# Optimization experiments

Hardware: AMD Instinct MI355X
Metric: run time of the kernel (lower is better)

## Reference

```python
import jax, jax.numpy as jnp
import numpy as np

B_SZ, L, D_MODEL = 8, 4096, 64
D_INNER, D_STATE, DT_RANK, K = 128, 16, 4, 4  # expand=2, d_state=16, dt_rank=ceil(64/16), d_conv=4


def setup_inputs() -> dict:
    key = jax.random.key(0)
    ks = jax.random.split(key, 8)
    r = lambda k, sh, s=0.02: jax.random.normal(k, sh, dtype=jnp.float32) * s
    A_init = jnp.log(jnp.arange(1, D_STATE + 1, dtype=jnp.float32))  # S4D-real init
    return {
        "x": jax.random.normal(ks[0], (B_SZ, L, D_MODEL), dtype=jnp.float32),
        "ln_g": jnp.ones((D_MODEL,), jnp.float32),
        "ln_b": jnp.zeros((D_MODEL,), jnp.float32),
        "in_proj_w": r(ks[1], (2, 2 * D_INNER, D_MODEL)),
        "conv_w": r(ks[2], (2, D_INNER, K), 0.1),
        "conv_b": jnp.zeros((2, D_INNER), jnp.float32),
        "x_proj_w": r(ks[3], (2, DT_RANK + 2 * D_STATE, D_INNER)),
        "dt_proj_w": r(ks[4], (2, D_INNER, DT_RANK), 0.1),
        "dt_bias": jnp.full((2, D_INNER), -4.0, jnp.float32) + r(ks[5], (2, D_INNER), 0.1),
        "A_log": jnp.broadcast_to(A_init, (2, D_INNER, D_STATE)) + 0.0,
        "D": jnp.ones((2, D_INNER), jnp.float32),
        "out_proj_w": r(ks[6], (2, D_MODEL, D_INNER)),
    }


def _mamba(x, in_w, cw, cb, xp_w, dtp_w, dtb, A_log, Dp, out_w):
    # x: [B, L, d_model] -> [B, L, d_model]
    xz = x @ in_w.T                         # [B, L, 2*d_inner]
    xi, z = jnp.split(xz, 2, axis=-1)
    # causal depthwise conv1d, kernel K, left-pad K-1
    xi_c = jnp.transpose(xi, (0, 2, 1))     # [B, d_inner, L]
    xi_c = jax.lax.conv_general_dilated(
        xi_c, cw[:, None, :], (1,), [(K - 1, 0)],
        dimension_numbers=("NCH", "OIH", "NCH"), feature_group_count=D_INNER)
    xi = jax.nn.silu(jnp.transpose(xi_c, (0, 2, 1)) + cb)  # [B, L, d_inner]
    xdb = xi @ xp_w.T                       # [B, L, dt_rank + 2*N]
    dt_low, Bm, C = jnp.split(xdb, [DT_RANK, DT_RANK + D_STATE], axis=-1)
    dt = jax.nn.softplus(dt_low @ dtp_w.T + dtb)  # [B, L, d_inner]
    A = -jnp.exp(A_log)                     # [d_inner, N]

    def step(h, inp):
        xt, dtt, Bt, Ct = inp               # [B,d], [B,d], [B,N], [B,N]
        dA = jnp.exp(dtt[..., None] * A)    # [B, d, N]
        h = dA * h + (dtt * xt)[..., None] * Bt[:, None, :]
        return h, jnp.einsum("bdn,bn->bd", h, Ct)

    h0 = jnp.zeros((x.shape[0], D_INNER, D_STATE), x.dtype)
    seq = (jnp.swapaxes(xi, 0, 1), jnp.swapaxes(dt, 0, 1),
           jnp.swapaxes(Bm, 0, 1), jnp.swapaxes(C, 0, 1))
    _, ys = jax.lax.scan(step, h0, seq)
    y = jnp.swapaxes(ys, 0, 1) + xi * Dp    # D skip connection
    y = y * jax.nn.silu(z)                  # gate
    return y @ out_w.T                      # [B, L, d_model]


def reference(x, ln_g, ln_b, in_proj_w, conv_w, conv_b, x_proj_w, dt_proj_w, dt_bias, A_log, D, out_proj_w):
    mu = jnp.mean(x, axis=-1, keepdims=True)
    var = jnp.var(x, axis=-1, keepdims=True)
    xn = (x - mu) * jax.lax.rsqrt(var + 1e-5) * ln_g + ln_b
    p = lambda i: (in_proj_w[i], conv_w[i], conv_b[i], x_proj_w[i], dt_proj_w[i],
                   dt_bias[i], A_log[i], D[i], out_proj_w[i])
    y_fwd = _mamba(xn, *p(0))
    y_bwd = jnp.flip(_mamba(jnp.flip(xn, axis=1), *p(1)), axis=1)
    return y_fwd + y_bwd
```

## Files before the change

### kernel.cpp

```cpp
#include <hip/hip_runtime.h>

#define Bsz 8
#define Lx 4096
#define DM 64
#define DI 128
#define NS 16
#define RK 4
#define KC 4
#define NC 64
#define CT 64

typedef __attribute__((ext_vector_type(8))) __bf16 bf16x8v;
typedef __attribute__((ext_vector_type(4))) __bf16 bf16x4v;
typedef __attribute__((ext_vector_type(4))) float f32x4;

__device__ __forceinline__ float fsig(float x){ return 1.f/(1.f+__expf(-x)); }
__device__ __forceinline__ float dot4(float4 a, float4 b){
  return fmaf(a.x,b.x, fmaf(a.y,b.y, fmaf(a.z,b.z, a.w*b.w)));
}
__device__ __forceinline__ void pow8(float e1, int half, float p[8]){
  float e2=e1*e1, e4=e2*e2, e8=e4*e4;
  if (half){
    p[0]=e8*e1; p[1]=e8*e2; p[2]=p[1]*e1; p[3]=e8*e4;
    p[4]=p[3]*e1; p[5]=p[3]*e2; p[6]=p[5]*e1; p[7]=e8*e8;
  } else {
    p[0]=e1; p[1]=e2; p[2]=e2*e1; p[3]=e4;
    p[4]=e4*e1; p[5]=e4*e2; p[6]=p[5]*e1; p[7]=e8;
  }
}

__global__ __launch_bounds__(512) void a1_front(
    const float* __restrict__ x, const float* __restrict__ ln_g, const float* __restrict__ ln_b,
    const float* __restrict__ in_w, const float* __restrict__ conv_w, const float* __restrict__ conv_b,
    const float* __restrict__ xp_w, const float* __restrict__ dtp_w, const float* __restrict__ dt_b,
    float* __restrict__ xcg, float* __restrict__ dtg, float* __restrict__ zg,
    float* __restrict__ Bg, float* __restrict__ Cg)
{
  __shared__ float uA[4864];
  __shared__ float uB[8192];
  const int tid = threadIdx.x;
  const int bx = blockIdx.x;
  const int tile = bx & 63;
  const int i = (bx >> 6) & 1;
  const int b = bx >> 7;
  const int l0 = tile * 64;
  const size_t rbase = (size_t)(b*2+i)*Lx + l0;

  {
    const int wv8 = tid >> 6, lane = tid & 63;
    const float gg = ln_g[lane], bb = ln_b[lane];
    for (int lr = wv8; lr < 67; lr += 8) {
      float v = 0.f;
      int l = l0 - 3 + lr;
      if (l >= 0) {
        int pl = i ? (Lx-1-l) : l;
        v = x[((size_t)b*Lx + pl)*DM + lane];
        float s = v, s2 = v*v;
        #pragma unroll
        for (int off=32; off; off>>=1){ s += __shfl_xor(s,off); s2 += __shfl_xor(s2,off); }
        float mu = s * (1.f/DM);
        float rs = rsqrtf(s2*(1.f/DM) - mu*mu + 1e-5f);
        v = (v-mu)*rs*gg + bb;
      }
      *(__bf16*)((char*)uA + ((lr*128 + lane*2) ^ ((lr&7)<<4))) = (__bf16)v;
    }
    #pragma unroll
    for (int it=0; it<8; ++it) {
      int g = it*512 + tid;
      int c = g >> 4, q = g & 15;
      float4 w = *(const float4*)(in_w + ((size_t)(i*2*DI) + c)*DM + q*4);
      bf16x4v hv;
      hv[0]=(__bf16)w.x; hv[1]=(__bf16)w.y; hv[2]=(__bf16)w.z; hv[3]=(__bf16)w.w;
      *(bf16x4v*)((char*)uB + ((c*128 + q*8) ^ ((c&7)<<4))) = hv;
    }
  }
  __syncthreads();

  const int lane = tid & 63, wv = tid >> 6;
  f32x4 acc[5][2];
  {
    f32x4 z4 = {0.f, 0.f, 0.f, 0.f};
    #pragma unroll
    for (int mt=0; mt<5; ++mt){ acc[mt][0] = z4; acc[mt][1] = z4; }
    bf16x8v bfr[2][2];
    #pragma unroll
    for (int ntl=0; ntl<2; ++ntl)
      #pragma unroll
      for (int kt=0; kt<2; ++kt){
        int c = (wv*2+ntl)*16 + (lane&15);
        int byt = (c*128 + kt*64 + (lane>>4)*16) ^ ((c&7)<<4);
        bfr[ntl][kt] = *(const bf16x8v*)((const char*)uB + byt);
      }
    #pragma unroll
    for (int mt=0; mt<5; ++mt){
      bf16x8v afr[2];
      #pragma unroll
      for (int kt=0; kt<2; ++kt){
        int row = mt*16 + (lane&15);
        int byt = (row*128 + kt*64 + (lane>>4)*16) ^ ((row&7)<<4);
        afr[kt] = *(const bf16x8v*)((const char*)uA + byt);
      }
      #pragma unroll
      for (int ntl=0; ntl<2; ++ntl){
        acc[mt][ntl] = __builtin_amdgcn_mfma_f32_16x16x32_bf16(afr[0], bfr[ntl][0], acc[mt][ntl], 0,0,0);
        acc[mt][ntl] = __builtin_amdgcn_mfma_f32_16x16x32_bf16(afr[1], bfr[ntl][1], acc[mt][ntl], 0,0,0);
      }
    }
  }
  __syncthreads();

  {
    const int d = tid & 127, rh = tid >> 7;
    const float4 cw = *(const float4*)(conv_w + (size_t)(i*DI + d)*KC);
    const float cb = conv_b[i*DI + d];
    #pragma unroll
    for (int h=0; h<2; ++h) {
      if (wv < 4) {
        #pragma unroll
        for (int mt=0; mt<5; ++mt)
          #pragma unroll
          for (int ntl=0; ntl<2; ++ntl)
            #pragma unroll
            for (int r=0; r<4; ++r){
              int m = mt*16 + (lane>>4)*4 + r;
              if (m >= h*32 && m <= h*32+34)
                uA[(m - h*32)*129 + wv*32 + ntl*16 + (lane&15)] = acc[mt][ntl][r];
            }
      } else if (h == 0) {
        #pragma unroll
        for (int mt=0; mt<5; ++mt)
          #pragma unroll
          for (int ntl=0; ntl<2; ++ntl)
            #pragma unroll
            for (int r=0; r<4; ++r){
              int m = mt*16 + (lane>>4)*4 + r;
              if (m >= 3 && m <= 66)
                zg[(rbase + (m-3))*DI + (wv-4)*32 + ntl*16 + (lane&15)] = acc[mt][ntl][r];
            }
      }
      __syncthreads();
      #pragma unroll
      for (int rr=0; rr<8; ++rr){
        int r = h*32 + rh*8 + rr;
        int lb = rh*8 + rr;
        float v0 = uA[(lb  )*129 + d];
        float v1 = uA[(lb+1)*129 + d];
        float v2 = uA[(lb+2)*129 + d];
        float v3 = uA[(lb+3)*129 + d];
        float aa = cb + cw.x*v0 + cw.y*v1 + cw.z*v2 + cw.w*v3;
        float xc = aa * fsig(aa);
        xcg[(rbase + r)*DI + d] = xc;
        __bf16 hh = (__bf16)xc;
        __bf16 ll = (__bf16)(xc - (float)hh);
        int off = (r*256 + d*2) ^ ((r&7)<<4);
        *(__bf16*)((char*)uB + off) = hh;
        *(__bf16*)((char*)uB + off + 16384) = ll;
      }
      __syncthreads();
    }
  }

  for (int e = tid; e < 36*32; e += 512) {
    int j = e >> 5, k0 = (e & 31)*4;
    float4 w = *(const float4*)(xp_w + ((size_t)(i*36) + j)*DI + k0);
    float vv[4] = {w.x, w.y, w.z, w.w};
    bf16x4v hv, lv;
    #pragma unroll
    for (int k=0;k<4;++k){
      __bf16 hh = (__bf16)vv[k];
      hv[k] = hh;
      lv[k] = (__bf16)(vv[k] - (float)hh);
    }
    int off = (j*256 + k0*2) ^ ((j&7)<<4);
    *(bf16x4v*)((char*)uA + off) = hv;
    *(bf16x4v*)((char*)uA + off + 9216) = lv;
  }
  __syncthreads();

  for (int t = wv; t < 12; t += 8) {
    int mt = t & 3, nt = t >> 2;
    f32x4 a2 = {0.f,0.f,0.f,0.f};
    #pragma unroll
    for (int kt=0; kt<4; ++kt){
      int row = mt*16 + (lane&15);
      int ab = (row*256 + kt*64 + (lane>>4)*16) ^ ((row&7)<<4);
      bf16x8v ah = *(const bf16x8v*)((const char*)uB + ab);
      bf16x8v al = *(const bf16x8v*)((const char*)uB + ab + 16384);
      int col = nt*16 + (lane&15);
      int bby = (col*256 + kt*64 + (lane>>4)*16) ^ ((col&7)<<4);
      bf16x8v bh = *(const bf16x8v*)((const char*)uA + bby);
      bf16x8v bl = *(const bf16x8v*)((const char*)uA + bby + 9216);
      a2 = __builtin_amdgcn_mfma_f32_16x16x32_bf16(ah, bh, a2, 0,0,0);
      a2 = __builtin_amdgcn_mfma_f32_16x16x32_bf16(al, bh, a2, 0,0,0);
      a2 = __builtin_amdgcn_mfma_f32_16x16x32_bf16(ah, bl, a2, 0,0,0);
    }
    #pragma unroll
    for (int rg4=0; rg4<4; ++rg4){
      int row = mt*16 + (lane>>4)*4 + rg4;
      int j = nt*16 + (lane&15);
      float val = a2[rg4];
      if (j < 4) uA[4608 + row*4 + j] = val;
      else if (j < 20) Bg[(rbase+row)*NS + (j-4)] = val;
      else if (j < 36) Cg[(rbase+row)*NS + (j-20)] = val;
    }
  }
  __syncthreads();

  #pragma unroll 4
  for (int it=0; it<16; ++it) {
    int e = it*512 + tid;
    int r = e >> 7, d = e & 127;
    float4 dl = *(const float4*)&uA[4608 + r*4];
    float4 w  = *(const float4*)(dtp_w + (size_t)(i*DI + d)*RK);
    float a = dt_b[i*DI + d] + dot4(w, dl);
    dtg[(rbase + r)*DI + d] = (a > 15.f) ? a : __logf(1.f + __expf(a));
  }
}

__global__ __launch_bounds__(256) void ks_scan(
    float* dtg, float* xcg,
    const float* __restrict__ Bg, const float* __restrict__ Cg,
    const float* __restrict__ A_log, const float* __restrict__ Dp,
    float* __restrict__ Pm, float* __restrict__ hend)
{
  __shared__ float sB[CT*NS];
  __shared__ float sC[CT*NS];
  const int tid = threadIdx.x;
  const int bx = blockIdx.x;
  const int c = bx % NC; const int i = (bx/NC)&1; const int b = bx/(2*NC);
  const int d = tid >> 1, half = tid & 1, n0 = half*8;
  const size_t rb = ((size_t)(b*2+i)*Lx + (size_t)c*CT);
  ((float4*)sB)[tid] = ((const float4*)(Bg + rb*NS))[tid];
  ((float4*)sC)[tid] = ((const float4*)(Cg + rb*NS))[tid];
  float a[8], h[8];
  bool afast = true;
  #pragma unroll
  for (int n=0;n<8;++n){
    a[n] = -__expf(A_log[((size_t)(i*DI)+d)*NS + n0+n]);
    float tgt = (float)(n0+n+1);
    afast = afast && (fabsf(a[n] + tgt) <= 1e-4f*tgt);
    h[n] = 0.f;
  }
  const float Dd = Dp[i*DI + d];
  float S = 0.f;
  float dt4[4], x4[4];
  #pragma unroll
  for (int k=0;k<4;++k){
    size_t g = (rb + k)*DI + d;
    dt4[k] = dtg[g];
    x4[k]  = xcg[g];
  }
  __syncthreads();
  for (int r4 = 0; r4 < CT; r4 += 4){
    float dtn[4], xn[4];
    if (r4 + 4 < CT){
      #pragma unroll
      for (int k=0;k<4;++k){
        size_t g = (rb + r4 + 4 + k)*DI + d;
        dtn[k] = dtg[g];
        xn[k]  = xcg[g];
      }
    }
    #pragma unroll
    for (int k=0;k<4;++k){
      float dtt = dt4[k];
      float xcv = x4[k];
      float u = dtt * xcv;
      S += dtt;
      const float* bp = &sB[(r4 + k)*NS + n0];
      const float* cp = &sC[(r4 + k)*NS + n0];
      float4 b0 = *(const float4*)bp;
      float4 b1 = *(const float4*)(bp+4);
      float4 c0 = *(const float4*)cp;
      float4 c1 = *(const float4*)(cp+4);
      float bb[8] = {b0.x,b0.y,b0.z,b0.w,b1.x,b1.y,b1.z,b1.w};
      float cc[8] = {c0.x,c0.y,c0.z,c0.w,c1.x,c1.y,c1.z,c1.w};
      float pA = 0.f, pB = 0.f;
      if (afast){
        float p[8];
        pow8(__expf(-dtt), half, p);
        #pragma unroll
        for (int n=0;n<8;++n){
          h[n] = fmaf(p[n], h[n], u*bb[n]);
          if (n & 1) pB = fmaf(h[n], cc[n], pB); else pA = fmaf(h[n], cc[n], pA);
        }
      } else {
        #pragma unroll
        for (int n=0;n<8;++n){
          float dA = __expf(a[n]*dtt);
          h[n] = fmaf(dA, h[n], u*bb[n]);
          if (n & 1) pB = fmaf(h[n], cc[n], pB); else pA = fmaf(h[n], cc[n], pA);
        }
      }
      float part = pA + pB;
      float y = part + __shfl_xor(part, 1);
      if (half == 0){
        size_t g = (rb + r4 + k)*DI + d;
        dtg[g] = fmaf(xcv, Dd, y);
        xcg[g] = S;
      }
    }
    if (r4 + 4 < CT){
      #pragma unroll
      for (int k=0;k<4;++k){ dt4[k] = dtn[k]; x4[k] = xn[k]; }
    }
  }
  size_t ob = (((size_t)(b*2+i)*NC + c)*DI + d)*NS + n0;
  if (afast){
    float p[8];
    pow8(__expf(-S), half, p);
    #pragma unroll
    for (int n=0;n<8;++n) Pm[ob+n] = p[n];
  } else {
    #pragma unroll
    for (int n=0;n<8;++n) Pm[ob+n] = __expf(a[n]*S);
  }
  #pragma unroll
  for (int n=0;n<8;++n) hend[ob+n] = h[n];
}

__global__ __launch_bounds__(256) void kc_pass2(
    float* __restrict__ Pm, const float* __restrict__ hend)
{
  const int tid = threadIdx.x;
  const int bi = blockIdx.x;
  const int d = tid>>1, n0 = (tid&1)*8;
  float h[8];
  #pragma unroll
  for (int n=0;n<8;++n) h[n]=0.f;
  const size_t stride = (size_t)DI*NS;
  size_t ob = (((size_t)bi*NC)*DI + d)*NS + n0;
  float4 pa = *(const float4*)&Pm[ob],   pb = *(const float4*)&Pm[ob+4];
  float4 ea = *(const float4*)&hend[ob], eb = *(const float4*)&hend[ob+4];
  for (int c=0; c<NC; ++c){
    size_t obn = ob + stride;
    float4 qa=pa, qb=pb, fa=ea, fb=eb;
    if (c+1 < NC){
      qa = *(const float4*)&Pm[obn];   qb = *(const float4*)&Pm[obn+4];
      fa = *(const float4*)&hend[obn]; fb = *(const float4*)&hend[obn+4];
    }
    *(float4*)&Pm[ob]   = make_float4(h[0],h[1],h[2],h[3]);
    *(float4*)&Pm[ob+4] = make_float4(h[4],h[5],h[6],h[7]);
    h[0]=fmaf(pa.x,h[0],ea.x); h[1]=fmaf(pa.y,h[1],ea.y);
    h[2]=fmaf(pa.z,h[2],ea.z); h[3]=fmaf(pa.w,h[3],ea.w);
    h[4]=fmaf(pb.x,h[4],eb.x); h[5]=fmaf(pb.y,h[5],eb.y);
    h[6]=fmaf(pb.z,h[6],eb.z); h[7]=fmaf(pb.w,h[7],eb.w);
    pa=qa; pb=qb; ea=fa; eb=fb; ob = obn;
  }
}

__global__ __launch_bounds__(256) void ke_out(
    const float* __restrict__ yg, const float* __restrict__ Sg,
    const float* __restrict__ zg, const float* __restrict__ Cg,
    const float* __restrict__ h0g, const float* __restrict__ A_log,
    const float* __restrict__ ow, float* __restrict__ out)
{
  __shared__ char sY[16384];
  __shared__ char sW[16384];
  int* s_af = (int*)sW;
  const int tid = threadIdx.x;
  const int bx = blockIdx.x;
  const int tile = bx & 127; const int b = bx >> 7;
  const int l0 = tile * 32;
  const int q = tid & 31, rg = tid >> 5;
  if (tid < 2) s_af[tid] = 1;
  bool bad0 = false, bad1 = false;
  #pragma unroll
  for (int it=0; it<8; ++it){
    int e = it*256 + tid;
    int n = e & 15;
    float tgt = (float)(n+1);
    float a0 = __expf(A_log[e]);
    float a1 = __expf(A_log[DI*NS + e]);
    if (fabsf(a0 - tgt) > 1e-4f*tgt) bad0 = true;
    if (fabsf(a1 - tgt) > 1e-4f*tgt) bad1 = true;
  }
  __syncthreads();
  if (bad0) s_af[0] = 0;
  if (bad1) s_af[1] = 0;
  __syncthreads();
  const bool af0 = (s_af[0] != 0), af1 = (s_af[1] != 0);
  #pragma unroll
  for (int dir=0; dir<2; ++dir){
    const size_t strm = (size_t)(b*2+dir);
    const int cch = dir ? ((Lx-1-l0)>>6) : (l0>>6);
    const bool afast = dir ? af1 : af0;
    float h0q[4][16];
    #pragma unroll
    for (int dd=0; dd<4; ++dd)
      #pragma unroll
      for (int k=0;k<4;++k)
        *(float4*)&h0q[dd][k*4] =
            *(const float4*)&h0g[(((strm*NC) + cch)*DI + (q*4+dd))*NS + k*4];
    #pragma unroll
    for (int it=0; it<4; ++it){
      int r = it*8 + rg;
      size_t prow = strm*Lx + (size_t)(dir ? (Lx-1-(l0+r)) : (l0+r));
      float4 y4 = *(const float4*)&yg[prow*DI + q*4];
      float4 S4 = *(const float4*)&Sg[prow*DI + q*4];
      float4 z4 = *(const float4*)&zg[prow*DI + q*4];
      float c16[16];
      #pragma unroll
      for (int k=0;k<4;++k) *(float4*)&c16[k*4] = *(const float4*)&Cg[prow*NS + k*4];
      float yv[4] = {y4.x,y4.y,y4.z,y4.w};
      float Sv[4] = {S4.x,S4.y,S4.z,S4.w};
      float zv[4] = {z4.x,z4.y,z4.z,z4.w};
      bf16x4v hv;
      #pragma unroll
      for (int dd=0; dd<4; ++dd){
        float corr;
        if (afast){
          float e1 = __expf(-Sv[dd]);
          float g[16];
          #pragma unroll
          for (int n=0;n<16;++n) g[n] = c16[n]*h0q[dd][n];
          float t = g[15];
          #pragma unroll
          for (int n=14;n>=0;--n) t = fmaf(t, e1, g[n]);
          corr = t * e1;
        } else {
          corr = 0.f;
          #pragma unroll
          for (int n=0;n<16;++n){
            float an = -__expf(A_log[((size_t)(dir*DI) + q*4+dd)*NS + n]);
            corr = fmaf(__expf(an*Sv[dd])*c16[n], h0q[dd][n], corr);
          }
        }
        float zz = zv[dd];
        float yf = (yv[dd] + corr) * (zz * fsig(zz));
        hv[dd] = (__bf16)yf;
      }
      *(bf16x4v*)(sY + ((r*512 + dir*256 + q*8) ^ ((r&7)<<4))) = hv;
    }
  }
  __syncthreads();
  const int lane = tid & 63, wv = tid >> 6;
  f32x4 acc2[2] = {{0.f,0.f,0.f,0.f},{0.f,0.f,0.f,0.f}};
  #pragma unroll
  for (int dir=0; dir<2; ++dir){
    #pragma unroll
    for (int it=0; it<8; ++it){
      int e = it*256 + tid;
      int c = e >> 5, qq = e & 31;
      float4 w = *(const float4*)(ow + ((size_t)(dir*DM + c))*DI + qq*4);
      bf16x4v hv; hv[0]=(__bf16)w.x; hv[1]=(__bf16)w.y; hv[2]=(__bf16)w.z; hv[3]=(__bf16)w.w;
      *(bf16x4v*)(sW + ((c*256 + qq*8) ^ ((c&7)<<4))) = hv;
    }
    __syncthreads();
    #pragma unroll
    for (int t=0; t<2; ++t){
      int T = wv*2 + t, mt = T >> 2, nt = T & 3;
      #pragma unroll
      for (int ktl=0; ktl<4; ++ktl){
        int row = mt*16 + (lane&15);
        bf16x8v av = *(const bf16x8v*)(sY + ((row*512 + dir*256 + ktl*64 + (lane>>4)*16) ^ ((row&7)<<4)));
        int ch = nt*16 + (lane&15);
        bf16x8v wvv = *(const bf16x8v*)(sW + ((ch*256 + ktl*64 + (lane>>4)*16) ^ ((ch&7)<<4)));
        acc2[t] = __builtin_amdgcn_mfma_f32_16x16x32_bf16(av, wvv, acc2[t], 0,0,0);
      }
    }
    __syncthreads();
  }
  #pragma unroll
  for (int t=0; t<2; ++t){
    int T = wv*2 + t, mt = T >> 2, nt = T & 3;
    #pragma unroll
    for (int r=0; r<4; ++r){
      int m = mt*16 + (lane>>4)*4 + r;
      int ch = nt*16 + (lane&15);
      out[((size_t)b*Lx + (size_t)(l0+m))*DM + ch] = acc2[t][r];
    }
  }
}

extern "C" void kernel_launch(void* const* d_in, const int* in_sizes, int n_in,
                              void* d_out, int out_size, void* d_ws, size_t ws_size,
                              hipStream_t stream)
{
  const float* x      = (const float*)d_in[0];
  const float* ln_g   = (const float*)d_in[1];
  const float* ln_b   = (const float*)d_in[2];
  const float* in_w   = (const float*)d_in[3];
  const float* conv_w = (const float*)d_in[4];
  const float* conv_b = (const float*)d_in[5];
  const float* xp_w   = (const float*)d_in[6];
  const float* dtp_w  = (const float*)d_in[7];
  const float* dt_b   = (const float*)d_in[8];
  const float* A_log  = (const float*)d_in[9];
  const float* Dp     = (const float*)d_in[10];
  const float* ow     = (const float*)d_in[11];
  float* out = (float*)d_out;
  float* ws = (float*)d_ws;
  const size_t NBD = (size_t)Bsz*2*Lx*DI;
  const size_t NBN = (size_t)Bsz*2*Lx*NS;
  float* xcg = ws;
  float* dtg = xcg + NBD;
  float* zg  = dtg + NBD;
  float* Bg  = zg + NBD;
  float* Cg  = Bg + NBN;
  float* Pm  = Cg + NBN;
  float* he  = out;

  a1_front<<<dim3(Bsz*2*(Lx/64)), dim3(512), 0, stream>>>(
      x, ln_g, ln_b, in_w, conv_w, conv_b, xp_w, dtp_w, dt_b, xcg, dtg, zg, Bg, Cg);
  ks_scan<<<dim3(Bsz*2*NC), dim3(256), 0, stream>>>(dtg, xcg, Bg, Cg, A_log, Dp, Pm, he);
  kc_pass2<<<dim3(Bsz*2), dim3(256), 0, stream>>>(Pm, he);
  ke_out<<<dim3(Bsz*(Lx/32)), dim3(256), 0, stream>>>(
      dtg, xcg, zg, Cg, Pm, A_log, ow, out);
}
```

Baseline: 133.4 us.

## Interleave dt/x buffers, split in_proj into two passes, drop low-bf16 x term

Stores dt and the conv output x interleaved as float2 in a single buffer. The scan now issues one 8-byte load per row instead of two scalar loads, and the output kernel reads y and S with paired float4 loads. The front kernel stages the in_proj weights in two halves to halve the uB LDS footprint, which may help occupancy but adds barriers. It also drops the low-order bf16 correction of x in the x_proj MFMA, trading some accuracy of dt/B/C for fewer MFMAs and less LDS.

```diff
diff --git a/kernel.cpp b/kernel.cpp
--- a/kernel.cpp
+++ b/kernel.cpp
@@ -33,11 +33,11 @@
     const float* __restrict__ x, const float* __restrict__ ln_g, const float* __restrict__ ln_b,
     const float* __restrict__ in_w, const float* __restrict__ conv_w, const float* __restrict__ conv_b,
     const float* __restrict__ xp_w, const float* __restrict__ dtp_w, const float* __restrict__ dt_b,
-    float* __restrict__ xcg, float* __restrict__ dtg, float* __restrict__ zg,
+    float* __restrict__ pxg, float* __restrict__ zg,
     float* __restrict__ Bg, float* __restrict__ Cg)
 {
   __shared__ float uA[4864];
-  __shared__ float uB[8192];
+  __shared__ float uB[4096];
   const int tid = threadIdx.x;
   const int bx = blockIdx.x;
   const int tile = bx & 63;
@@ -45,11 +45,11 @@
   const int b = bx >> 7;
   const int l0 = tile * 64;
   const size_t rbase = (size_t)(b*2+i)*Lx + l0;
+  const int lane = tid & 63, wv = tid >> 6;
 
   {
-    const int wv8 = tid >> 6, lane = tid & 63;
     const float gg = ln_g[lane], bb = ln_b[lane];
-    for (int lr = wv8; lr < 67; lr += 8) {
+    for (int lr = wv; lr < 67; lr += 8) {
       float v = 0.f;
       int l = l0 - 3 + lr;
       if (l >= 0) {
@@ -64,97 +64,88 @@
       }
       *(__bf16*)((char*)uA + ((lr*128 + lane*2) ^ ((lr&7)<<4))) = (__bf16)v;
     }
-    #pragma unroll
-    for (int it=0; it<8; ++it) {
-      int g = it*512 + tid;
-      int c = g >> 4, q = g & 15;
-      float4 w = *(const float4*)(in_w + ((size_t)(i*2*DI) + c)*DM + q*4);
-      bf16x4v hv;
-      hv[0]=(__bf16)w.x; hv[1]=(__bf16)w.y; hv[2]=(__bf16)w.z; hv[3]=(__bf16)w.w;
-      *(bf16x4v*)((char*)uB + ((c*128 + q*8) ^ ((c&7)<<4))) = hv;
-    }
-  }
-  __syncthreads();
-
-  const int lane = tid & 63, wv = tid >> 6;
+  }
+  __syncthreads();
+
   f32x4 acc[5][2];
   {
-    f32x4 z4 = {0.f, 0.f, 0.f, 0.f};
-    #pragma unroll
-    for (int mt=0; mt<5; ++mt){ acc[mt][0] = z4; acc[mt][1] = z4; }
-    bf16x8v bfr[2][2];
-    #pragma unroll
-    for (int ntl=0; ntl<2; ++ntl)
+    f32x4 z4v = {0.f, 0.f, 0.f, 0.f};
+    #pragma unroll
+    for (int mt=0; mt<5; ++mt){ acc[mt][0] = z4v; acc[mt][1] = z4v; }
+    #pragma unroll
+    for (int p = 0; p < 2; ++p) {
+      #pragma unroll
+      for (int it=0; it<4; ++it) {
+        int g = it*512 + tid;
+        int c = g >> 4, q = g & 15;
+        float4 w = *(const float4*)(in_w + ((size_t)(i*2*DI) + p*DI + c)*DM + q*4);
+        bf16x4v hv;
+        hv[0]=(__bf16)w.x; hv[1]=(__bf16)w.y; hv[2]=(__bf16)w.z; hv[3]=(__bf16)w.w;
+        *(bf16x4v*)((char*)uB + ((c*128 + q*8) ^ ((c&7)<<4))) = hv;
+      }
+      __syncthreads();
+      bf16x8v bfr[2];
       #pragma unroll
       for (int kt=0; kt<2; ++kt){
-        int c = (wv*2+ntl)*16 + (lane&15);
-        int byt = (c*128 + kt*64 + (lane>>4)*16) ^ ((c&7)<<4);
-        bfr[ntl][kt] = *(const bf16x8v*)((const char*)uB + byt);
-      }
-    #pragma unroll
-    for (int mt=0; mt<5; ++mt){
-      bf16x8v afr[2];
-      #pragma unroll
-      for (int kt=0; kt<2; ++kt){
-        int row = mt*16 + (lane&15);
-        int byt = (row*128 + kt*64 + (lane>>4)*16) ^ ((row&7)<<4);
-        afr[kt] = *(const bf16x8v*)((const char*)uA + byt);
-      }
-      #pragma unroll
-      for (int ntl=0; ntl<2; ++ntl){
-        acc[mt][ntl] = __builtin_amdgcn_mfma_f32_16x16x32_bf16(afr[0], bfr[ntl][0], acc[mt][ntl], 0,0,0);
-        acc[mt][ntl] = __builtin_amdgcn_mfma_f32_16x16x32_bf16(afr[1], bfr[ntl][1], acc[mt][ntl], 0,0,0);
-      }
-    }
-  }
-  __syncthreads();
+        int cl = wv*16 + (lane&15);
+        int byt = (cl*128 + kt*64 + (lane>>4)*16) ^ ((cl&7)<<4);
+        bfr[kt] = *(const bf16x8v*)((const char*)uB + byt);
+      }
+      #pragma unroll
+      for (int mt=0; mt<5; ++mt){
+        bf16x8v afr[2];
+        #pragma unroll
+        for (int kt=0; kt<2; ++kt){
+          int row = mt*16 + (lane&15);
+          int byt = (row*128 + kt*64 + (lane>>4)*16) ^ ((row&7)<<4);
+          afr[kt] = *(const bf16x8v*)((const char*)uA + byt);
+        }
+        acc[mt][p] = __builtin_amdgcn_mfma_f32_16x16x32_bf16(afr[0], bfr[0], acc[mt][p], 0,0,0);
+        acc[mt][p] = __builtin_amdgcn_mfma_f32_16x16x32_bf16(afr[1], bfr[1], acc[mt][p], 0,0,0);
+      }
+      __syncthreads();
+    }
+  }
 
   {
+    const int d0 = wv*16 + (lane&15);
     const int d = tid & 127, rh = tid >> 7;
     const float4 cw = *(const float4*)(conv_w + (size_t)(i*DI + d)*KC);
     const float cb = conv_b[i*DI + d];
     #pragma unroll
     for (int h=0; h<2; ++h) {
-      if (wv < 4) {
+      #pragma unroll
+      for (int mt=0; mt<5; ++mt)
+        #pragma unroll
+        for (int r=0; r<4; ++r){
+          int m = mt*16 + (lane>>4)*4 + r;
+          if (m >= h*32 && m <= h*32+34)
+            uA[(m - h*32)*129 + d0] = acc[mt][0][r];
+        }
+      if (h == 0) {
         #pragma unroll
         for (int mt=0; mt<5; ++mt)
           #pragma unroll
-          for (int ntl=0; ntl<2; ++ntl)
-            #pragma unroll
-            for (int r=0; r<4; ++r){
-              int m = mt*16 + (lane>>4)*4 + r;
-              if (m >= h*32 && m <= h*32+34)
-                uA[(m - h*32)*129 + wv*32 + ntl*16 + (lane&15)] = acc[mt][ntl][r];
-            }
-      } else if (h == 0) {
-        #pragma unroll
-        for (int mt=0; mt<5; ++mt)
-          #pragma unroll
-          for (int ntl=0; ntl<2; ++ntl)
-            #pragma unroll
-            for (int r=0; r<4; ++r){
-              int m = mt*16 + (lane>>4)*4 + r;
-              if (m >= 3 && m <= 66)
-                zg[(rbase + (m-3))*DI + (wv-4)*32 + ntl*16 + (lane&15)] = acc[mt][ntl][r];
-            }
+          for (int r=0; r<4; ++r){
+            int m = mt*16 + (lane>>4)*4 + r;
+            if (m >= 3 && m <= 66)
+              zg[(rbase + (m-3))*DI + d0] = acc[mt][1][r];
+          }
       }
       __syncthreads();
       #pragma unroll
       for (int rr=0; rr<8; ++rr){
-        int r = h*32 + rh*8 + rr;
         int lb = rh*8 + rr;
+        int r = h*32 + lb;
         float v0 = uA[(lb  )*129 + d];
         float v1 = uA[(lb+1)*129 + d];
         float v2 = uA[(lb+2)*129 + d];
         float v3 = uA[(lb+3)*129 + d];
         float aa = cb + cw.x*v0 + cw.y*v1 + cw.z*v2 + cw.w*v3;
         float xc = aa * fsig(aa);
-        xcg[(rbase + r)*DI + d] = xc;
-        __bf16 hh = (__bf16)xc;
-        __bf16 ll = (__bf16)(xc - (float)hh);
+        pxg[((rbase + r)*DI + d)*2 + 1] = xc;
         int off = (r*256 + d*2) ^ ((r&7)<<4);
-        *(__bf16*)((char*)uB + off) = hh;
-        *(__bf16*)((char*)uB + off + 16384) = ll;
+        *(__bf16*)((char*)uB + off) = (__bf16)xc;
       }
       __syncthreads();
     }
@@ -185,13 +176,11 @@
       int row = mt*16 + (lane&15);
       int ab = (row*256 + kt*64 + (lane>>4)*16) ^ ((row&7)<<4);
       bf16x8v ah = *(const bf16x8v*)((const char*)uB + ab);
-      bf16x8v al = *(const bf16x8v*)((const char*)uB + ab + 16384);
       int col = nt*16 + (lane&15);
       int bby = (col*256 + kt*64 + (lane>>4)*16) ^ ((col&7)<<4);
       bf16x8v bh = *(const bf16x8v*)((const char*)uA + bby);
       bf16x8v bl = *(const bf16x8v*)((const char*)uA + bby + 9216);
       a2 = __builtin_amdgcn_mfma_f32_16x16x32_bf16(ah, bh, a2, 0,0,0);
-      a2 = __builtin_amdgcn_mfma_f32_16x16x32_bf16(al, bh, a2, 0,0,0);
       a2 = __builtin_amdgcn_mfma_f32_16x16x32_bf16(ah, bl, a2, 0,0,0);
     }
     #pragma unroll
@@ -213,12 +202,12 @@
     float4 dl = *(const float4*)&uA[4608 + r*4];
     float4 w  = *(const float4*)(dtp_w + (size_t)(i*DI + d)*RK);
     float a = dt_b[i*DI + d] + dot4(w, dl);
-    dtg[(rbase + r)*DI + d] = (a > 15.f) ? a : __logf(1.f + __expf(a));
+    pxg[((rbase + r)*DI + d)*2] = (a > 15.f) ? a : __logf(1.f + __expf(a));
   }
 }
 
 __global__ __launch_bounds__(256) void ks_scan(
-    float* dtg, float* xcg,
+    float* pxg,
     const float* __restrict__ Bg, const float* __restrict__ Cg,
     const float* __restrict__ A_log, const float* __restrict__ Dp,
     float* __restrict__ Pm, float* __restrict__ hend)
@@ -232,6 +221,7 @@
   const size_t rb = ((size_t)(b*2+i)*Lx + (size_t)c*CT);
   ((float4*)sB)[tid] = ((const float4*)(Bg + rb*NS))[tid];
   ((float4*)sC)[tid] = ((const float4*)(Cg + rb*NS))[tid];
+  float2* px2 = (float2*)pxg;
   float a[8], h[8];
   bool afast = true;
   #pragma unroll
@@ -243,28 +233,20 @@
   }
   const float Dd = Dp[i*DI + d];
   float S = 0.f;
-  float dt4[4], x4[4];
-  #pragma unroll
-  for (int k=0;k<4;++k){
-    size_t g = (rb + k)*DI + d;
-    dt4[k] = dtg[g];
-    x4[k]  = xcg[g];
-  }
+  float2 cur[4];
+  #pragma unroll
+  for (int k=0;k<4;++k) cur[k] = px2[(rb + k)*DI + d];
   __syncthreads();
   for (int r4 = 0; r4 < CT; r4 += 4){
-    float dtn[4], xn[4];
+    float2 nxt[4];
     if (r4 + 4 < CT){
       #pragma unroll
-      for (int k=0;k<4;++k){
-        size_t g = (rb + r4 + 4 + k)*DI + d;
-        dtn[k] = dtg[g];
-        xn[k]  = xcg[g];
-      }
+      for (int k=0;k<4;++k) nxt[k] = px2[(rb + r4 + 4 + k)*DI + d];
     }
     #pragma unroll
     for (int k=0;k<4;++k){
-      float dtt = dt4[k];
-      float xcv = x4[k];
+      float dtt = cur[k].x;
+      float xcv = cur[k].y;
       float u = dtt * xcv;
       S += dtt;
       const float* bp = &sB[(r4 + k)*NS + n0];
@@ -294,15 +276,12 @@
       }
       float part = pA + pB;
       float y = part + __shfl_xor(part, 1);
-      if (half == 0){
-        size_t g = (rb + r4 + k)*DI + d;
-        dtg[g] = fmaf(xcv, Dd, y);
-        xcg[g] = S;
-      }
+      if (half == 0)
+        px2[(rb + r4 + k)*DI + d] = make_float2(fmaf(xcv, Dd, y), S);
     }
     if (r4 + 4 < CT){
       #pragma unroll
-      for (int k=0;k<4;++k){ dt4[k] = dtn[k]; x4[k] = xn[k]; }
+      for (int k=0;k<4;++k) cur[k] = nxt[k];
     }
   }
   size_t ob = (((size_t)(b*2+i)*NC + c)*DI + d)*NS + n0;
@@ -350,7 +329,7 @@
 }
 
 __global__ __launch_bounds__(256) void ke_out(
-    const float* __restrict__ yg, const float* __restrict__ Sg,
+    const float* __restrict__ pxg,
     const float* __restrict__ zg, const float* __restrict__ Cg,
     const float* __restrict__ h0g, const float* __restrict__ A_log,
     const float* __restrict__ ow, float* __restrict__ out)
@@ -396,15 +375,15 @@
     for (int it=0; it<4; ++it){
       int r = it*8 + rg;
       size_t prow = strm*Lx + (size_t)(dir ? (Lx-1-(l0+r)) : (l0+r));
-      float4 y4 = *(const float4*)&yg[prow*DI + q*4];
-      float4 S4 = *(const float4*)&Sg[prow*DI + q*4];
+      const float4* p4 = (const float4*)(pxg + (prow*DI + q*4)*2);
+      float4 ya = p4[0], yb = p4[1];
       float4 z4 = *(const float4*)&zg[prow*DI + q*4];
       float c16[16];
       #pragma unroll
       for (int k=0;k<4;++k) *(float4*)&c16[k*4] = *(const float4*)&Cg[prow*NS + k*4];
-      float yv[4] = {y4.x,y4.y,y4.z,y4.w};
-      float Sv[4] = {S4.x,S4.y,S4.z,S4.w};
-      float zv[4] = {z4.x,z4.y,z4.z,z4.w};
+      float yv[4] = {ya.x, ya.z, yb.x, yb.z};
+      float Sv[4] = {ya.y, ya.w, yb.y, yb.w};
+      float zv[4] = {z4.x, z4.y, z4.z, z4.w};
       bf16x4v hv;
       #pragma unroll
       for (int dd=0; dd<4; ++dd){
@@ -493,18 +472,17 @@
   float* ws = (float*)d_ws;
   const size_t NBD = (size_t)Bsz*2*Lx*DI;
   const size_t NBN = (size_t)Bsz*2*Lx*NS;
-  float* xcg = ws;
-  float* dtg = xcg + NBD;
-  float* zg  = dtg + NBD;
+  float* pxg = ws;
+  float* zg  = pxg + 2*NBD;
   float* Bg  = zg + NBD;
   float* Cg  = Bg + NBN;
   float* Pm  = Cg + NBN;
   float* he  = out;
 
   a1_front<<<dim3(Bsz*2*(Lx/64)), dim3(512), 0, stream>>>(
-      x, ln_g, ln_b, in_w, conv_w, conv_b, xp_w, dtp_w, dt_b, xcg, dtg, zg, Bg, Cg);
-  ks_scan<<<dim3(Bsz*2*NC), dim3(256), 0, stream>>>(dtg, xcg, Bg, Cg, A_log, Dp, Pm, he);
+      x, ln_g, ln_b, in_w, conv_w, conv_b, xp_w, dtp_w, dt_b, pxg, zg, Bg, Cg);
+  ks_scan<<<dim3(Bsz*2*NC), dim3(256), 0, stream>>>(pxg, Bg, Cg, A_log, Dp, Pm, he);
   kc_pass2<<<dim3(Bsz*2), dim3(256), 0, stream>>>(Pm, he);
   ke_out<<<dim3(Bsz*(Lx/32)), dim3(256), 0, stream>>>(
-      dtg, xcg, zg, Cg, Pm, A_log, ow, out);
-}
+      pxg, zg, Cg, Pm, A_log, ow, out);
+}
```

Result: slower. 140.8 us (+5.5%).

## Halve front-kernel LDS by staging in_proj weights in two passes and dropping xc low part

Applied to the files above, without the earlier changes.

The in_proj weight tile is now staged into shared memory in two halves (x part, then z part), so the uB buffer shrinks from 32KB to 16KB. Each wave now computes one 16-column slice per half instead of two slices at once. The low-order bf16 correction term of the conv output is dropped from the x_proj split-precision MFMA, which removes one MFMA per k-step and its LDS storage. The goal is lower LDS use for higher occupancy and less work. The cost is extra barriers and lower precision in the B/C/dt projection.

```diff
diff --git a/kernel.cpp b/kernel.cpp
--- a/kernel.cpp
+++ b/kernel.cpp
@@ -37,7 +37,7 @@
     float* __restrict__ Bg, float* __restrict__ Cg)
 {
   __shared__ float uA[4864];
-  __shared__ float uB[8192];
+  __shared__ float uB[4096];
   const int tid = threadIdx.x;
   const int bx = blockIdx.x;
   const int tile = bx & 63;
@@ -45,11 +45,11 @@
   const int b = bx >> 7;
   const int l0 = tile * 64;
   const size_t rbase = (size_t)(b*2+i)*Lx + l0;
+  const int lane = tid & 63, wv = tid >> 6;
 
   {
-    const int wv8 = tid >> 6, lane = tid & 63;
     const float gg = ln_g[lane], bb = ln_b[lane];
-    for (int lr = wv8; lr < 67; lr += 8) {
+    for (int lr = wv; lr < 67; lr += 8) {
       float v = 0.f;
       int l = l0 - 3 + lr;
       if (l >= 0) {
@@ -64,85 +64,79 @@
       }
       *(__bf16*)((char*)uA + ((lr*128 + lane*2) ^ ((lr&7)<<4))) = (__bf16)v;
     }
-    #pragma unroll
-    for (int it=0; it<8; ++it) {
-      int g = it*512 + tid;
-      int c = g >> 4, q = g & 15;
-      float4 w = *(const float4*)(in_w + ((size_t)(i*2*DI) + c)*DM + q*4);
-      bf16x4v hv;
-      hv[0]=(__bf16)w.x; hv[1]=(__bf16)w.y; hv[2]=(__bf16)w.z; hv[3]=(__bf16)w.w;
-      *(bf16x4v*)((char*)uB + ((c*128 + q*8) ^ ((c&7)<<4))) = hv;
-    }
-  }
-  __syncthreads();
-
-  const int lane = tid & 63, wv = tid >> 6;
+  }
+  __syncthreads();
+
   f32x4 acc[5][2];
   {
-    f32x4 z4 = {0.f, 0.f, 0.f, 0.f};
-    #pragma unroll
-    for (int mt=0; mt<5; ++mt){ acc[mt][0] = z4; acc[mt][1] = z4; }
-    bf16x8v bfr[2][2];
-    #pragma unroll
-    for (int ntl=0; ntl<2; ++ntl)
+    f32x4 z4v = {0.f, 0.f, 0.f, 0.f};
+    #pragma unroll
+    for (int mt=0; mt<5; ++mt){ acc[mt][0] = z4v; acc[mt][1] = z4v; }
+    #pragma unroll
+    for (int p = 0; p < 2; ++p) {
+      #pragma unroll
+      for (int it=0; it<4; ++it) {
+        int g = it*512 + tid;
+        int c = g >> 4, q = g & 15;
+        float4 w = *(const float4*)(in_w + ((size_t)(i*2*DI) + p*DI + c)*DM + q*4);
+        bf16x4v hv;
+        hv[0]=(__bf16)w.x; hv[1]=(__bf16)w.y; hv[2]=(__bf16)w.z; hv[3]=(__bf16)w.w;
+        *(bf16x4v*)((char*)uB + ((c*128 + q*8) ^ ((c&7)<<4))) = hv;
+      }
+      __syncthreads();
+      bf16x8v bfr[2];
       #pragma unroll
       for (int kt=0; kt<2; ++kt){
-        int c = (wv*2+ntl)*16 + (lane&15);
-        int byt = (c*128 + kt*64 + (lane>>4)*16) ^ ((c&7)<<4);
-        bfr[ntl][kt] = *(const bf16x8v*)((const char*)uB + byt);
-      }
-    #pragma unroll
-    for (int mt=0; mt<5; ++mt){
-      bf16x8v afr[2];
-      #pragma unroll
-      for (int kt=0; kt<2; ++kt){
-        int row = mt*16 + (lane&15);
-        int byt = (row*128 + kt*64 + (lane>>4)*16) ^ ((row&7)<<4);
-        afr[kt] = *(const bf16x8v*)((const char*)uA + byt);
-      }
-      #pragma unroll
-      for (int ntl=0; ntl<2; ++ntl){
-        acc[mt][ntl] = __builtin_amdgcn_mfma_f32_16x16x32_bf16(afr[0], bfr[ntl][0], acc[mt][ntl], 0,0,0);
-        acc[mt][ntl] = __builtin_amdgcn_mfma_f32_16x16x32_bf16(afr[1], bfr[ntl][1], acc[mt][ntl], 0,0,0);
-      }
-    }
-  }
-  __syncthreads();
+        int cl = wv*16 + (lane&15);
+        int byt = (cl*128 + kt*64 + (lane>>4)*16) ^ ((cl&7)<<4);
+        bfr[kt] = *(const bf16x8v*)((const char*)uB + byt);
+      }
+      #pragma unroll
+      for (int mt=0; mt<5; ++mt){
+        bf16x8v afr[2];
+        #pragma unroll
+        for (int kt=0; kt<2; ++kt){
+          int row = mt*16 + (lane&15);
+          int byt = (row*128 + kt*64 + (lane>>4)*16) ^ ((row&7)<<4);
+          afr[kt] = *(const bf16x8v*)((const char*)uA + byt);
+        }
+        acc[mt][p] = __builtin_amdgcn_mfma_f32_16x16x32_bf16(afr[0], bfr[0], acc[mt][p], 0,0,0);
+        acc[mt][p] = __builtin_amdgcn_mfma_f32_16x16x32_bf16(afr[1], bfr[1], acc[mt][p], 0,0,0);
+      }
+      __syncthreads();
+    }
+  }
 
   {
+    const int d0 = wv*16 + (lane&15);
     const int d = tid & 127, rh = tid >> 7;
     const float4 cw = *(const float4*)(conv_w + (size_t)(i*DI + d)*KC);
     const float cb = conv_b[i*DI + d];
     #pragma unroll
     for (int h=0; h<2; ++h) {
-      if (wv < 4) {
+      #pragma unroll
+      for (int mt=0; mt<5; ++mt)
+        #pragma unroll
+        for (int r=0; r<4; ++r){
+          int m = mt*16 + (lane>>4)*4 + r;
+          if (m >= h*32 && m <= h*32+34)
+            uA[(m - h*32)*129 + d0] = acc[mt][0][r];
+        }
+      if (h == 0) {
         #pragma unroll
         for (int mt=0; mt<5; ++mt)
           #pragma unroll
-          for (int ntl=0; ntl<2; ++ntl)
-            #pragma unroll
-            for (int r=0; r<4; ++r){
-              int m = mt*16 + (lane>>4)*4 + r;
-              if (m >= h*32 && m <= h*32+34)
-                uA[(m - h*32)*129 + wv*32 + ntl*16 + (lane&15)] = acc[mt][ntl][r];
-            }
-      } else if (h == 0) {
-        #pragma unroll
-        for (int mt=0; mt<5; ++mt)
-          #pragma unroll
-          for (int ntl=0; ntl<2; ++ntl)
-            #pragma unroll
-            for (int r=0; r<4; ++r){
-              int m = mt*16 + (lane>>4)*4 + r;
-              if (m >= 3 && m <= 66)
-                zg[(rbase + (m-3))*DI + (wv-4)*32 + ntl*16 + (lane&15)] = acc[mt][ntl][r];
-            }
+          for (int r=0; r<4; ++r){
+            int m = mt*16 + (lane>>4)*4 + r;
+            if (m >= 3 && m <= 66)
+              zg[(rbase + (m-3))*DI + d0] = acc[mt][1][r];
+          }
       }
       __syncthreads();
       #pragma unroll
       for (int rr=0; rr<8; ++rr){
-        int r = h*32 + rh*8 + rr;
         int lb = rh*8 + rr;
+        int r = h*32 + lb;
         float v0 = uA[(lb  )*129 + d];
         float v1 = uA[(lb+1)*129 + d];
         float v2 = uA[(lb+2)*129 + d];
@@ -150,11 +144,8 @@
         float aa = cb + cw.x*v0 + cw.y*v1 + cw.z*v2 + cw.w*v3;
         float xc = aa * fsig(aa);
         xcg[(rbase + r)*DI + d] = xc;
-        __bf16 hh = (__bf16)xc;
-        __bf16 ll = (__bf16)(xc - (float)hh);
         int off = (r*256 + d*2) ^ ((r&7)<<4);
-        *(__bf16*)((char*)uB + off) = hh;
-        *(__bf16*)((char*)uB + off + 16384) = ll;
+        *(__bf16*)((char*)uB + off) = (__bf16)xc;
       }
       __syncthreads();
     }
@@ -185,13 +176,11 @@
       int row = mt*16 + (lane&15);
       int ab = (row*256 + kt*64 + (lane>>4)*16) ^ ((row&7)<<4);
       bf16x8v ah = *(const bf16x8v*)((const char*)uB + ab);
-      bf16x8v al = *(const bf16x8v*)((const char*)uB + ab + 16384);
       int col = nt*16 + (lane&15);
       int bby = (col*256 + kt*64 + (lane>>4)*16) ^ ((col&7)<<4);
       bf16x8v bh = *(const bf16x8v*)((const char*)uA + bby);
       bf16x8v bl = *(const bf16x8v*)((const char*)uA + bby + 9216);
       a2 = __builtin_amdgcn_mfma_f32_16x16x32_bf16(ah, bh, a2, 0,0,0);
-      a2 = __builtin_amdgcn_mfma_f32_16x16x32_bf16(al, bh, a2, 0,0,0);
       a2 = __builtin_amdgcn_mfma_f32_16x16x32_bf16(ah, bl, a2, 0,0,0);
     }
     #pragma unroll
```

New measurement: 130.6 us. -2.1%, faster.
